# Performance work log

Measured on AMD Instinct MI355X. Metric: run time of the kernel, lower is better.

The kernel has to match this reference:

```python
import jax, jax.numpy as jnp
import numpy as np

N = 100000   # number of points
K = 256      # num_clusters
F = 256      # num_features


def setup_inputs() -> dict:
    key = jax.random.key(0)
    k1, k2 = jax.random.split(key)
    x = jax.random.normal(k1, (1, N, F), dtype=jnp.float32)
    cluster_centers = jax.random.normal(k2, (K, F), dtype=jnp.float32)
    return {"x": x, "cluster_centers": cluster_centers}


def reference(x, cluster_centers):
    # x: (1, n, F); cluster_centers: (K, F)
    # Euclidean distances (1, n, K) via expansion (same math as norm of diff,
    # without materializing the (1, n, K, F) intermediate the torch code builds).
    x_sq = jnp.sum(x * x, axis=-1)                              # (1, n)
    c_sq = jnp.sum(cluster_centers * cluster_centers, axis=-1)  # (K,)
    cross = jnp.einsum('bnf,kf->bnk', x, cluster_centers)       # (1, n, K)
    d2 = x_sq[..., None] + c_sq[None, None, :] - 2.0 * cross
    distances = jnp.sqrt(jnp.maximum(d2, 0.0))                  # (1, n, K)
    # For each cluster, index of the nearest point (argmin over n).
    indices = jnp.argmin(distances, axis=1)                     # (1, K)
    # Gather the features of the nearest point per cluster.
    selected = jnp.take_along_axis(x, indices[:, :, None], axis=1)  # (1, K, F)
    return selected
```

## Files before the change

### kernel.cpp

```cpp
#include <hip/hip_runtime.h>
#include <stdint.h>

#define N_PTS 100000
#define K_CL  256
#define F_DIM 256
#define LDSPAD 40

using bf16x8 = __attribute__((ext_vector_type(8))) short;
using f32x4  = __attribute__((ext_vector_type(4))) float;
typedef unsigned long long u64;

__device__ __forceinline__ unsigned short f32_to_bf16_rne(float f) {
    unsigned u = __float_as_uint(f);
    unsigned r = u + 0x7FFFu + ((u >> 16) & 1u);
    return (unsigned short)(r >> 16);
}

__global__ void prep_kernel(const float* __restrict__ c,
                            unsigned short* __restrict__ ch,
                            unsigned short* __restrict__ cl,
                            float* __restrict__ csq,
                            u64* __restrict__ best) {
    const int k = blockIdx.x;
    const int lane = threadIdx.x;
    float4 v = *(const float4*)(c + (size_t)k * F_DIM + lane * 4);

    float e[4] = {v.x, v.y, v.z, v.w};
    unsigned short hh[4], ll[4];
    #pragma unroll
    for (int i = 0; i < 4; ++i) {
        hh[i] = f32_to_bf16_rne(e[i]);
        float hf = __uint_as_float((unsigned)hh[i] << 16);
        ll[i] = f32_to_bf16_rne(e[i] - hf);
    }
    *(ushort4*)(ch + (size_t)k * F_DIM + lane * 4) = make_ushort4(hh[0], hh[1], hh[2], hh[3]);
    *(ushort4*)(cl + (size_t)k * F_DIM + lane * 4) = make_ushort4(ll[0], ll[1], ll[2], ll[3]);

    float s = v.x * v.x;
    s = fmaf(v.y, v.y, s);
    s = fmaf(v.z, v.z, s);
    s = fmaf(v.w, v.w, s);
    #pragma unroll
    for (int off = 32; off; off >>= 1) s += __shfl_down(s, off, 64);
    if (lane == 0) { csq[k] = s; best[k] = 0xFFFFFFFFFFFFFFFFULL; }
}

__global__ __launch_bounds__(512, 4)
void cluster_argmin_kernel(const float* __restrict__ x,
                           const unsigned short* __restrict__ ch,
                           const unsigned short* __restrict__ cl,
                           const float* __restrict__ csq,
                           u64* __restrict__ best) {
    __shared__ unsigned short xh_lds[2][64][LDSPAD];
    __shared__ unsigned short xl_lds[2][64][LDSPAD];
    __shared__ float xsq_lds[64];

    const int tid  = threadIdx.x;
    const int lane = tid & 63;
    const int w    = __builtin_amdgcn_readfirstlane(tid >> 6);
    const int kb   = w * 32;
    const int n0   = blockIdx.x * 64;
    const int r15  = lane & 15;
    const int kg   = lane >> 4;

    const int cp = tid >> 3;
    const int cc = tid & 7;
    int nrow = n0 + cp; if (nrow > N_PTS - 1) nrow = N_PTS - 1;
    const float* xptr = x + (size_t)nrow * F_DIM + cc * 4;

    const unsigned short* cbh[2];
    const unsigned short* cbl[2];
    #pragma unroll
    for (int cg = 0; cg < 2; ++cg) {
        size_t off = (size_t)(kb + cg * 16 + r15) * F_DIM + kg * 8;
        cbh[cg] = ch + off;
        cbl[cg] = cl + off;
    }

    f32x4 acc[4][2];
    #pragma unroll
    for (int pg = 0; pg < 4; ++pg)
        #pragma unroll
        for (int cg = 0; cg < 2; ++cg)
            acc[pg][cg] = (f32x4){0.f, 0.f, 0.f, 0.f};
    float xsq_p = 0.f;

    float4 nxt = *(const float4*)(xptr);
    #pragma unroll 1
    for (int it = 0; it < 8; ++it) {
        const int f0 = it * 32;
        unsigned short h4[4], l4[4];
        float e[4] = {nxt.x, nxt.y, nxt.z, nxt.w};
        #pragma unroll
        for (int i = 0; i < 4; ++i) {
            h4[i] = f32_to_bf16_rne(e[i]);
            float hf = __uint_as_float((unsigned)h4[i] << 16);
            l4[i] = f32_to_bf16_rne(e[i] - hf);
            xsq_p = fmaf(e[i], e[i], xsq_p);
        }
        if (it < 7) nxt = *(const float4*)(xptr + (it + 1) * 32);

        *(ushort4*)&xh_lds[it & 1][cp][cc * 4] = make_ushort4(h4[0], h4[1], h4[2], h4[3]);
        *(ushort4*)&xl_lds[it & 1][cp][cc * 4] = make_ushort4(l4[0], l4[1], l4[2], l4[3]);

        bf16x8 bh[2], bl[2];
        #pragma unroll
        for (int cg = 0; cg < 2; ++cg) {
            bh[cg] = *(const bf16x8*)(cbh[cg] + f0);
            bl[cg] = *(const bf16x8*)(cbl[cg] + f0);
        }
        __syncthreads();

        #pragma unroll
        for (int pg = 0; pg < 4; ++pg) {
            bf16x8 xh8 = *(const bf16x8*)&xh_lds[it & 1][pg * 16 + r15][kg * 8];
            bf16x8 xl8 = *(const bf16x8*)&xl_lds[it & 1][pg * 16 + r15][kg * 8];
            #pragma unroll
            for (int cg = 0; cg < 2; ++cg) {
                acc[pg][cg] = __builtin_amdgcn_mfma_f32_16x16x32_bf16(
                    xh8, bh[cg], acc[pg][cg], 0, 0, 0);
                acc[pg][cg] = __builtin_amdgcn_mfma_f32_16x16x32_bf16(
                    xh8, bl[cg], acc[pg][cg], 0, 0, 0);
                acc[pg][cg] = __builtin_amdgcn_mfma_f32_16x16x32_bf16(
                    xl8, bh[cg], acc[pg][cg], 0, 0, 0);
            }
        }
    }

    xsq_p += __shfl_xor(xsq_p, 1, 64);
    xsq_p += __shfl_xor(xsq_p, 2, 64);
    xsq_p += __shfl_xor(xsq_p, 4, 64);
    if (cc == 0) xsq_lds[cp] = xsq_p;
    __syncthreads();

    u64 keep = 0xFFFFFFFFFFFFFFFFULL;
    #pragma unroll
    for (int cg = 0; cg < 2; ++cg) {
        const float cs = csq[kb + cg * 16 + r15];
        u64 m = 0xFFFFFFFFFFFFFFFFULL;
        #pragma unroll
        for (int pg = 0; pg < 4; ++pg) {
            #pragma unroll
            for (int r = 0; r < 4; ++r) {
                const int pl = pg * 16 + kg * 4 + r;
                const int n  = n0 + pl;
                float d2 = fmaf(-2.f, acc[pg][cg][r], xsq_lds[pl] + cs);
                d2 = fmaxf(d2, 0.f);
                float d = sqrtf(d2);
                u64 pk = ((u64)__float_as_uint(d) << 32) | (unsigned)n;
                if (n >= N_PTS) pk = 0xFFFFFFFFFFFFFFFFULL;
                m = pk < m ? pk : m;
            }
        }
        u64 o = __shfl_xor(m, 16, 64); m = o < m ? o : m;
        o = __shfl_xor(m, 32, 64);     m = o < m ? o : m;
        if (kg == cg) keep = m;
    }
    if (lane < 32) {
        u64 cur = best[kb + lane];
        if (keep < cur) atomicMin(&best[kb + lane], keep);
    }
}

__global__ void gather_kernel(const float* __restrict__ x,
                              const u64* __restrict__ best,
                              float* __restrict__ out) {
    int k = blockIdx.x;
    unsigned int idx = (unsigned int)(best[k] & 0xFFFFFFFFULL);
    int t = threadIdx.x;
    float4 v = *(const float4*)(x + (size_t)idx * F_DIM + t * 4);
    *(float4*)(out + (size_t)k * F_DIM + t * 4) = v;
}

extern "C" void kernel_launch(void* const* d_in, const int* in_sizes, int n_in,
                              void* d_out, int out_size, void* d_ws, size_t ws_size,
                              hipStream_t stream) {
    const float* x = (const float*)d_in[0];
    const float* c = (const float*)d_in[1];
    float* out = (float*)d_out;

    u64* best  = (u64*)d_ws;
    float* csq = (float*)((char*)d_ws + K_CL * sizeof(u64));

    unsigned short* ch = (unsigned short*)d_out;
    unsigned short* cl = ch + (size_t)K_CL * F_DIM;

    prep_kernel<<<K_CL, 64, 0, stream>>>(c, ch, cl, csq, best);

    int nblocks = (N_PTS + 63) / 64;
    cluster_argmin_kernel<<<nblocks, 512, 0, stream>>>(x, ch, cl, csq, best);

    gather_kernel<<<K_CL, 64, 0, stream>>>(x, best, out);
}
```

Baseline: 210.9 us.

## Stage full 64-point x tile into LDS upfront, drop per-iteration barriers

Instead of streaming x in 32-feature chunks through a double-buffered LDS with a barrier on every iteration, each wave first loads, splits to bf16 hi/lo, and stores whole rows of the 64-point tile into a full-width LDS buffer. It also computes row norms with a wave reduction, then issues a single barrier. The MFMA loop then runs barrier-free with unroll 2. This removes eight block syncs and the interleaved conversion work, at the cost of about 67KB LDS per block, which may limit occupancy below the declared 4 blocks per CU, and it loses the load/compute overlap.

```diff
diff --git a/kernel.cpp b/kernel.cpp
--- a/kernel.cpp
+++ b/kernel.cpp
@@ -4,7 +4,7 @@
 #define N_PTS 100000
 #define K_CL  256
 #define F_DIM 256
-#define LDSPAD 40
+#define XROW  264
 
 using bf16x8 = __attribute__((ext_vector_type(8))) short;
 using f32x4  = __attribute__((ext_vector_type(4))) float;
@@ -51,23 +51,42 @@
                            const unsigned short* __restrict__ cl,
                            const float* __restrict__ csq,
                            u64* __restrict__ best) {
-    __shared__ unsigned short xh_lds[2][64][LDSPAD];
-    __shared__ unsigned short xl_lds[2][64][LDSPAD];
+    __shared__ unsigned short xh_lds[64][XROW];
+    __shared__ unsigned short xl_lds[64][XROW];
     __shared__ float xsq_lds[64];
 
     const int tid  = threadIdx.x;
     const int lane = tid & 63;
     const int w    = __builtin_amdgcn_readfirstlane(tid >> 6);
-    const int kb   = w * 32;
     const int n0   = blockIdx.x * 64;
     const int r15  = lane & 15;
     const int kg   = lane >> 4;
 
-    const int cp = tid >> 3;
-    const int cc = tid & 7;
-    int nrow = n0 + cp; if (nrow > N_PTS - 1) nrow = N_PTS - 1;
-    const float* xptr = x + (size_t)nrow * F_DIM + cc * 4;
+    const int col = lane * 4;
+    #pragma unroll
+    for (int i = 0; i < 8; ++i) {
+        const int row = w + i * 8;
+        int gr = n0 + row; if (gr > N_PTS - 1) gr = N_PTS - 1;
+        float4 v = *(const float4*)(x + (size_t)gr * F_DIM + col);
+        unsigned short h4[4], l4[4];
+        float e[4] = {v.x, v.y, v.z, v.w};
+        float s = 0.f;
+        #pragma unroll
+        for (int j = 0; j < 4; ++j) {
+            h4[j] = f32_to_bf16_rne(e[j]);
+            float hf = __uint_as_float((unsigned)h4[j] << 16);
+            l4[j] = f32_to_bf16_rne(e[j] - hf);
+            s = fmaf(e[j], e[j], s);
+        }
+        *(ushort4*)&xh_lds[row][col] = make_ushort4(h4[0], h4[1], h4[2], h4[3]);
+        *(ushort4*)&xl_lds[row][col] = make_ushort4(l4[0], l4[1], l4[2], l4[3]);
+        #pragma unroll
+        for (int off = 32; off; off >>= 1) s += __shfl_xor(s, off, 64);
+        if (lane == 0) xsq_lds[row] = s;
+    }
+    __syncthreads();
 
+    const int kb = w * 32;
     const unsigned short* cbh[2];
     const unsigned short* cbl[2];
     #pragma unroll
@@ -83,38 +102,20 @@
         #pragma unroll
         for (int cg = 0; cg < 2; ++cg)
             acc[pg][cg] = (f32x4){0.f, 0.f, 0.f, 0.f};
-    float xsq_p = 0.f;
 
-    float4 nxt = *(const float4*)(xptr);
-    #pragma unroll 1
+    #pragma unroll 2
     for (int it = 0; it < 8; ++it) {
         const int f0 = it * 32;
-        unsigned short h4[4], l4[4];
-        float e[4] = {nxt.x, nxt.y, nxt.z, nxt.w};
-        #pragma unroll
-        for (int i = 0; i < 4; ++i) {
-            h4[i] = f32_to_bf16_rne(e[i]);
-            float hf = __uint_as_float((unsigned)h4[i] << 16);
-            l4[i] = f32_to_bf16_rne(e[i] - hf);
-            xsq_p = fmaf(e[i], e[i], xsq_p);
-        }
-        if (it < 7) nxt = *(const float4*)(xptr + (it + 1) * 32);
-
-        *(ushort4*)&xh_lds[it & 1][cp][cc * 4] = make_ushort4(h4[0], h4[1], h4[2], h4[3]);
-        *(ushort4*)&xl_lds[it & 1][cp][cc * 4] = make_ushort4(l4[0], l4[1], l4[2], l4[3]);
-
         bf16x8 bh[2], bl[2];
         #pragma unroll
         for (int cg = 0; cg < 2; ++cg) {
             bh[cg] = *(const bf16x8*)(cbh[cg] + f0);
             bl[cg] = *(const bf16x8*)(cbl[cg] + f0);
         }
-        __syncthreads();
-
         #pragma unroll
         for (int pg = 0; pg < 4; ++pg) {
-            bf16x8 xh8 = *(const bf16x8*)&xh_lds[it & 1][pg * 16 + r15][kg * 8];
-            bf16x8 xl8 = *(const bf16x8*)&xl_lds[it & 1][pg * 16 + r15][kg * 8];
+            bf16x8 xh8 = *(const bf16x8*)&xh_lds[pg * 16 + r15][f0 + kg * 8];
+            bf16x8 xl8 = *(const bf16x8*)&xl_lds[pg * 16 + r15][f0 + kg * 8];
             #pragma unroll
             for (int cg = 0; cg < 2; ++cg) {
                 acc[pg][cg] = __builtin_amdgcn_mfma_f32_16x16x32_bf16(
@@ -126,12 +127,6 @@
             }
         }
     }
-
-    xsq_p += __shfl_xor(xsq_p, 1, 64);
-    xsq_p += __shfl_xor(xsq_p, 2, 64);
-    xsq_p += __shfl_xor(xsq_p, 4, 64);
-    if (cc == 0) xsq_lds[cp] = xsq_p;
-    __syncthreads();
 
     u64 keep = 0xFFFFFFFFFFFFFFFFULL;
     #pragma unroll
```

Result: slower. 217.4 us (+3.1%).
